# Optimization experiments

Hardware: AMD Instinct MI355X
Metric: run time of the kernel (lower is better)

Reference implementation:

```python
import jax, jax.numpy as jnp
import numpy as np

B, S, DM, H = 4, 1024, 1024, 16
DK = DM // H  # 64, must equal embeddim=64

def _linear(x, W, b):
    # torch nn.Linear: y = x @ W.T + b, W is [out, in]
    return jnp.matmul(x, W.T) + b

def setup_inputs() -> dict:
    key = jax.random.key(0)
    ks = jax.random.split(key, 40)
    inp = {}
    inp["query"] = jax.random.normal(ks[0], (B, S, DM), jnp.float32)
    inp["key"] = jax.random.normal(ks[1], (B, S, DM), jnp.float32)
    inp["value"] = jax.random.normal(ks[2], (B, S, DM), jnp.float32)
    inp["mask"] = jnp.ones((B, S, S), jnp.int32)
    def mk(i, dout, din):
        W = jax.random.normal(ks[i], (dout, din), jnp.float32) / np.sqrt(din).astype(np.float32)
        b = jax.random.normal(ks[i + 20], (dout,), jnp.float32) * 0.01
        return W, b
    # the 4 d_model x d_model projection linears (q, k, v, out)
    inp["Wq"], inp["bq"] = mk(3, DM, DM)
    inp["Wk"], inp["bk"] = mk(4, DM, DM)
    inp["Wv"], inp["bv"] = mk(5, DM, DM)
    inp["Wo"], inp["bo"] = mk(6, DM, DM)
    # the 64x64 refinement linears
    inp["Wkl"], inp["bkl"] = mk(7, DK, DK)   # key_linear
    inp["Wql"], inp["bql"] = mk(8, DK, DK)   # query_linear
    inp["Wq2"], inp["bq2"] = mk(9, DK, DK)   # query2_linear
    inp["Wvl"], inp["bvl"] = mk(10, DK, DK)  # value_linear
    inp["Wel"], inp["bel"] = mk(11, DK, DK)  # embed_linear
    return inp

def reference(query, key, value, mask,
              Wq, bq, Wk, bk, Wv, bv, Wo, bo,
              Wkl, bkl, Wql, bql, Wq2, bq2, Wvl, bvl, Wel, bel):
    b, s, dm = query.shape
    # project and split heads: [b, h, s, d_k]
    def split(x):
        return x.reshape(b, s, H, DK).transpose(0, 2, 1, 3)
    q = split(_linear(query, Wq, bq))
    k = split(_linear(key, Wk, bk))
    v = split(_linear(value, Wv, bv))
    # per-head 64x64 refinements with relu
    key_refine = jax.nn.relu(_linear(k, Wkl, bkl))
    q1 = jax.nn.relu(_linear(q, Wql, bql))
    q1 = jax.nn.relu(_linear(q1, Wel, bel))
    q2 = jax.nn.relu(_linear(q, Wq2, bq2))
    v_refine = jax.nn.relu(_linear(v, Wvl, bvl))
    # two attention-like matmuls (no 1/sqrt(d_k) scaling in original)
    qv = jnp.einsum("bhqd,bhkd->bhqk", q2, v_refine)
    kq = jnp.einsum("bhqd,bhkd->bhqk", q1, key_refine)
    m = mask[:, None, :, :]  # mask.unsqueeze(1)
    kq = jnp.where(m == 0, jnp.float32(-1e9), kq)
    attn = jax.nn.softmax(kq, axis=-1)
    # elementwise combine, then matmul against raw projected key (not value!)
    out = jnp.einsum("bhqk,bhkd->bhqd", attn * qv, k)
    out = out.transpose(0, 2, 1, 3).reshape(b, s, dm)
    return _linear(out, Wo, bo)
```

## Files before the change

kernel.cpp:

```cpp
#include <hip/hip_runtime.h>
#include <hip/hip_bf16.h>

#define B_  4
#define S_  1024
#define DM_ 1024
#define H_  16
#define DK_ 64
#define LOG2E 1.4426950408889634f

typedef unsigned short u16;
typedef __attribute__((ext_vector_type(8))) short bf16x8;
typedef __attribute__((ext_vector_type(4))) float f32x4;

__device__ __forceinline__ float bf2f(u16 u) {
    union { unsigned int i; float f; } c;
    c.i = ((unsigned int)u) << 16;
    return c.f;
}
__device__ __forceinline__ u16 f2bf(float f) {
    union { float f; unsigned int i; } c;
    c.f = f;
    unsigned int x = c.i;
    unsigned int lsb = (x >> 16) & 1u;
    x += 0x7fffu + lsb;
    return (u16)(x >> 16);
}
__device__ __forceinline__ u16 f2bf_fast(float f) {
    __hip_bfloat16 h = __float2bfloat16(f);
    return *reinterpret_cast<u16*>(&h);
}

__device__ __forceinline__ void async_ld16(const u16* g, u16* l) {
    __builtin_amdgcn_global_load_lds(
        (const __attribute__((address_space(1))) unsigned int*)(const void*)g,
        (__attribute__((address_space(3))) unsigned int*)(void*)l, 16, 0, 0);
}

__global__ void detect_kernel(const u16* __restrict__ q, int* __restrict__ flag) {
    int lane = threadIdx.x & 63;
    int cnt = 0;
#pragma unroll
    for (int i = 0; i < 4; ++i) {
        u16 u = q[2 * (lane * 4 + i)];
        int e = (u >> 7) & 0xFF;
        cnt += (e >= 100 && e <= 140) ? 1 : 0;
    }
#pragma unroll
    for (int off = 1; off < 64; off <<= 1) cnt += __shfl_xor(cnt, off, 64);
    if (lane == 0) *flag = (cnt < 128) ? 1 : 0;
}

#define NSEG 12
struct CvtArgs {
    const void* src[NSEG];
    void*       dst[NSEG];
    unsigned    off[NSEG + 1];
};

__global__ __launch_bounds__(256) void convert_kernel(
    CvtArgs a, unsigned total, const int* __restrict__ flag)
{
    if (!*flag) return;
    unsigned v = blockIdx.x * 256 + threadIdx.x;
    if (v >= total) return;
    int s = 0;
    while (s < NSEG - 1 && v >= a.off[s + 1]) ++s;
    unsigned local = v - a.off[s];
    u16* dp = (u16*)a.dst[s] + (size_t)local * 8;
    const float* sp = (const float*)a.src[s] + (size_t)local * 8;
    float4 x = *(const float4*)sp, y = *(const float4*)(sp + 4);
    u16 t[8] = {f2bf(x.x), f2bf(x.y), f2bf(x.z), f2bf(x.w),
                f2bf(y.x), f2bf(y.y), f2bf(y.z), f2bf(y.w)};
    *(uint4*)dp = *(uint4*)t;
}

__global__ __launch_bounds__(256) void maskflag_kernel(
    const int* __restrict__ mask, int* __restrict__ tflags)
{
    const int kt = blockIdx.x, b = blockIdx.y, z = blockIdx.z;
    const int tid = threadIdx.x;
    int ok = 1;
#pragma unroll
    for (int i = tid; i < 128 * 16; i += 256) {
        int row = z * 128 + (i >> 4), seg = i & 15;
        int4 m = *(const int4*)&mask[((size_t)b * S_ + row) * S_ + kt * 64 + seg * 4];
        ok &= (m.x != 0) & (m.y != 0) & (m.z != 0) & (m.w != 0);
    }
    if (!ok) atomicOr(&tflags[b * 16 + kt], 1);
}

__global__ __launch_bounds__(256) void transpose_kernel(
    const u16* __restrict__ kp, u16* __restrict__ kpt)
{
    __shared__ u16 T[64][65];
    const int s0 = blockIdx.x * 64, h = blockIdx.y, b = blockIdx.z;
    const int tid = threadIdx.x;
    const size_t base = (size_t)b * S_ * DM_ + (size_t)h * DK_;
    for (int c = tid; c < 512; c += 256) {
        int row = c >> 3, cc = (c & 7) * 8;
        union { uint4 v; u16 u[8]; } x;
        x.v = *(const uint4*)&kp[base + (size_t)(s0 + row) * DM_ + cc];
#pragma unroll
        for (int j = 0; j < 8; ++j) T[row][cc + j] = x.u[j];
    }
    __syncthreads();
    const size_t baseT = (size_t)(b * H_ + h) * DK_ * S_;
    for (int c = tid; c < 512; c += 256) {
        int d = c >> 3, ss = (c & 7) * 8;
        u16 t[8];
#pragma unroll
        for (int j = 0; j < 8; ++j) t[j] = T[ss + j][d];
        *(uint4*)&kpt[baseT + (size_t)d * S_ + s0 + ss] = *(uint4*)t;
    }
}

struct GemmBatch {
    const u16* A0[4]; const u16* A1[4];
    const u16* W0[4]; const u16* W1[4];
    const void* bias[4];
    void* C[4];
    float oscale[4];
};

template<int ACT, int BIAS_DYN, int OUT_DYN>
__global__ __launch_bounds__(256, 3) void gemm_async_kernel(
    GemmBatch gb, int M, int N, int K, const int* __restrict__ flag)
{
    __shared__ __align__(16) u16 As[128][64];
    __shared__ __align__(16) u16 Ws[128][64];

    const int g = blockIdx.z;
    const int f = *flag;
    const u16* __restrict__ A = f ? gb.A1[g] : gb.A0[g];
    const u16* __restrict__ W = f ? gb.W1[g] : gb.W0[g];
    const void* biasp = gb.bias[g];
    void* Cp = gb.C[g];

    const int m0   = blockIdx.y * 128;
    const int n0   = blockIdx.x * 128;
    const int tid  = threadIdx.x;
    const int w    = tid >> 6;
    const int lane = tid & 63;
    const int l16  = lane & 15;
    const int quad = lane >> 4;
    const int wr   = (w >> 1) * 64;
    const int wc   = (w & 1) * 64;

    const int srow = lane >> 3;
    const int sgrp = (lane & 7) ^ srow;

    f32x4 acc[4][4];
#pragma unroll
    for (int rt = 0; rt < 4; ++rt)
#pragma unroll
        for (int ct = 0; ct < 4; ++ct) acc[rt][ct] = (f32x4){0.f, 0.f, 0.f, 0.f};

    for (int k0 = 0; k0 < K; k0 += 64) {
#pragma unroll
        for (int s = 0; s < 4; ++s) {
            int seg = w * 4 + s;
            async_ld16(&A[(size_t)(m0 + seg * 8 + srow) * K + k0 + sgrp * 8],
                       &As[seg * 8][0]);
            async_ld16(&W[(size_t)(n0 + seg * 8 + srow) * K + k0 + sgrp * 8],
                       &Ws[seg * 8][0]);
        }
        __syncthreads();
#pragma unroll
        for (int kk = 0; kk < 2; ++kk) {
            const int p = (kk * 4 + quad) ^ (l16 & 7);
            bf16x8 av[4], bv[4];
#pragma unroll
            for (int rt = 0; rt < 4; ++rt)
                av[rt] = *(const bf16x8*)&As[wr + rt * 16 + l16][p * 8];
#pragma unroll
            for (int ct = 0; ct < 4; ++ct)
                bv[ct] = *(const bf16x8*)&Ws[wc + ct * 16 + l16][p * 8];
#pragma unroll
            for (int rt = 0; rt < 4; ++rt)
#pragma unroll
                for (int ct = 0; ct < 4; ++ct)
                    acc[rt][ct] = __builtin_amdgcn_mfma_f32_16x16x32_bf16(
                        av[rt], bv[ct], acc[rt][ct], 0, 0, 0);
        }
        __syncthreads();
    }

#pragma unroll
    for (int ct = 0; ct < 4; ++ct) {
        int col = n0 + wc + ct * 16 + l16;
        float bv = (BIAS_DYN && f) ? ((const float*)biasp)[col]
                                   : bf2f(((const u16*)biasp)[col]);
#pragma unroll
        for (int rt = 0; rt < 4; ++rt)
#pragma unroll
            for (int r = 0; r < 4; ++r) {
                int row = m0 + wr + rt * 16 + quad * 4 + r;
                float v = acc[rt][ct][r] + bv;
                if (ACT) v = v > 0.f ? v : 0.f;
                size_t idx = (size_t)row * N + col;
                if (OUT_DYN && f) ((float*)Cp)[idx] = v;
                else              ((u16*)Cp)[idx]   = f2bf(v);
            }
    }
}

template<int ACT, int BIAS_DYN, int OUT_DYN>
__global__ __launch_bounds__(256, 2) void gemm_small_kernel(
    GemmBatch gb, int M, int N, int K, const int* __restrict__ flag)
{
    __shared__ __align__(16) u16 As[128][72];
    __shared__ __align__(16) u16 Ws[64][72];

    const int g = blockIdx.z;
    const int f = *flag;
    const u16* __restrict__ A = f ? gb.A1[g] : gb.A0[g];
    const u16* __restrict__ W = f ? gb.W1[g] : gb.W0[g];
    const void* biasp = gb.bias[g];
    void* Cp = gb.C[g];
    const float osc = gb.oscale[g];

    const int m0   = blockIdx.y * 128;
    const int n0   = blockIdx.x * 64;
    const int tid  = threadIdx.x;
    const int w    = tid >> 6;
    const int lane = tid & 63;
    const int l16  = lane & 15;
    const int quad = lane >> 4;

    f32x4 acc[2][4];
#pragma unroll
    for (int rt = 0; rt < 2; ++rt)
#pragma unroll
        for (int ct = 0; ct < 4; ++ct) acc[rt][ct] = (f32x4){0.f, 0.f, 0.f, 0.f};

    for (int k0 = 0; k0 < K; k0 += 64) {
#pragma unroll
        for (int c = tid; c < 1024; c += 256) {
            int row = c >> 3, cc = (c & 7) * 8;
            *(uint4*)&As[row][cc] = *(const uint4*)&A[(size_t)(m0 + row) * K + k0 + cc];
        }
#pragma unroll
        for (int c = tid; c < 512; c += 256) {
            int row = c >> 3, cc = (c & 7) * 8;
            *(uint4*)&Ws[row][cc] = *(const uint4*)&W[(size_t)(n0 + row) * K + k0 + cc];
        }
        __syncthreads();
#pragma unroll
        for (int kk = 0; kk < 2; ++kk) {
            bf16x8 a[2], b[4];
#pragma unroll
            for (int rt = 0; rt < 2; ++rt)
                a[rt] = *(const bf16x8*)&As[w * 32 + rt * 16 + l16][kk * 32 + quad * 8];
#pragma unroll
            for (int ct = 0; ct < 4; ++ct)
                b[ct] = *(const bf16x8*)&Ws[ct * 16 + l16][kk * 32 + quad * 8];
#pragma unroll
            for (int rt = 0; rt < 2; ++rt)
#pragma unroll
                for (int ct = 0; ct < 4; ++ct)
                    acc[rt][ct] = __builtin_amdgcn_mfma_f32_16x16x32_bf16(
                        a[rt], b[ct], acc[rt][ct], 0, 0, 0);
        }
        __syncthreads();
    }

#pragma unroll
    for (int ct = 0; ct < 4; ++ct) {
        int col = n0 + ct * 16 + l16;
        float bv = (BIAS_DYN && f) ? ((const float*)biasp)[col]
                                   : bf2f(((const u16*)biasp)[col]);
#pragma unroll
        for (int rt = 0; rt < 2; ++rt)
#pragma unroll
            for (int r = 0; r < 4; ++r) {
                int row = m0 + w * 32 + rt * 16 + quad * 4 + r;
                float v = acc[rt][ct][r] + bv;
                if (ACT) v = v > 0.f ? v : 0.f;
                v *= osc;
                size_t idx = (size_t)row * N + col;
                if (OUT_DYN && f) ((float*)Cp)[idx] = v;
                else              ((u16*)Cp)[idx]   = f2bf(v);
            }
    }
}

__global__ __launch_bounds__(256, 2) void attn_kernel(
    const u16* __restrict__ q1, const u16* __restrict__ q2,
    const u16* __restrict__ kr, const u16* __restrict__ vr,
    const u16* __restrict__ kpt, const int* __restrict__ mask,
    const int* __restrict__ tflags, u16* __restrict__ om)
{
    __shared__ __align__(16) u16 kbuf[2][3][64][64];
    __shared__ __align__(16) u16 pts[4][32][72];

    const int qt   = blockIdx.x;
    const int h    = blockIdx.y;
    const int b    = blockIdx.z;
    const int q0   = qt * 128;
    const int tid  = threadIdx.x;
    const int w    = tid >> 6;
    const int lane = tid & 63;
    const int l16  = lane & 15;
    const int quad = lane >> 4;
    const int pb   = l16 & 7;

    const size_t base  = (size_t)b * S_ * DM_ + (size_t)h * DK_;
    const size_t baseT = (size_t)(b * H_ + h) * DK_ * S_;

    const int srow = lane >> 3;
    const int sgrp = (lane & 7) ^ srow;

    auto stage = [&](int kt, int bsel) {
        const int k0 = kt * 64;
#pragma unroll
        for (int j = 0; j < 6; ++j) {
            int idx = w * 6 + j;
            int t = idx >> 3, s = idx & 7;
            const u16* g;
            if (t == 0)      g = &kr[base + (size_t)(k0 + s * 8 + srow) * DM_ + sgrp * 8];
            else if (t == 1) g = &vr[base + (size_t)(k0 + s * 8 + srow) * DM_ + sgrp * 8];
            else             g = &kpt[baseT + (size_t)(s * 8 + srow) * S_ + k0 + sgrp * 8];
            async_ld16(g, &kbuf[bsel][t][s * 8][0]);
        }
    };

    bf16x8 a1[2][2], a2[2][2];
#pragma unroll
    for (int rt = 0; rt < 2; ++rt) {
        const int qrow = q0 + w * 32 + rt * 16 + l16;
#pragma unroll
        for (int kk = 0; kk < 2; ++kk) {
            a1[rt][kk] = *(const bf16x8*)&q1[base + (size_t)qrow * DM_ + kk * 32 + quad * 8];
            a2[rt][kk] = *(const bf16x8*)&q2[base + (size_t)qrow * DM_ + kk * 32 + quad * 8];
        }
    }

    float m_run[2][4], l_run[2][4];
    f32x4 oacc[2][4];
#pragma unroll
    for (int rt = 0; rt < 2; ++rt)
#pragma unroll
        for (int r = 0; r < 4; ++r) { m_run[rt][r] = -1e30f; l_run[rt][r] = 0.f; }
#pragma unroll
    for (int rt = 0; rt < 2; ++rt)
#pragma unroll
        for (int ct = 0; ct < 4; ++ct) oacc[rt][ct] = (f32x4){0.f, 0.f, 0.f, 0.f};

    stage(0, 0);

    for (int kt = 0; kt < S_ / 64; ++kt) {
        const int cur = kt & 1;
        const int k0 = kt * 64;
        __syncthreads();
        if (kt < S_ / 64 - 1) stage(kt + 1, cur ^ 1);

        const int tf = tflags[b * 16 + kt];

        f32x4 s1[2][4], s2[2][4];
#pragma unroll
        for (int rt = 0; rt < 2; ++rt)
#pragma unroll
            for (int ct = 0; ct < 4; ++ct) {
                s1[rt][ct] = (f32x4){0.f, 0.f, 0.f, 0.f};
                s2[rt][ct] = (f32x4){0.f, 0.f, 0.f, 0.f};
            }
#pragma unroll
        for (int kk = 0; kk < 2; ++kk) {
            bf16x8 b1[4], b2[4];
#pragma unroll
            for (int ct = 0; ct < 4; ++ct) {
                const int p = (kk * 4 + quad) ^ pb;
                b1[ct] = *(const bf16x8*)&kbuf[cur][0][ct * 16 + l16][p * 8];
                b2[ct] = *(const bf16x8*)&kbuf[cur][1][ct * 16 + l16][p * 8];
            }
#pragma unroll
            for (int rt = 0; rt < 2; ++rt)
#pragma unroll
                for (int ct = 0; ct < 4; ++ct) {
                    s1[rt][ct] = __builtin_amdgcn_mfma_f32_16x16x32_bf16(
                        a1[rt][kk], b1[ct], s1[rt][ct], 0, 0, 0);
                    s2[rt][ct] = __builtin_amdgcn_mfma_f32_16x16x32_bf16(
                        a2[rt][kk], b2[ct], s2[rt][ct], 0, 0, 0);
                }
        }

        if (tf) {
#pragma unroll
            for (int rt = 0; rt < 2; ++rt)
#pragma unroll
                for (int ct = 0; ct < 4; ++ct)
#pragma unroll
                    for (int r = 0; r < 4; ++r) {
                        int qrow = q0 + w * 32 + rt * 16 + quad * 4 + r;
                        int kc   = k0 + ct * 16 + l16;
                        if (mask[((size_t)b * S_ + qrow) * S_ + kc] == 0)
                            s1[rt][ct][r] = -1e9f;
                    }
        }

        float tmax[2][4];
#pragma unroll
        for (int rt = 0; rt < 2; ++rt)
#pragma unroll
            for (int r = 0; r < 4; ++r) tmax[rt][r] = -1e30f;
#pragma unroll
        for (int rt = 0; rt < 2; ++rt)
#pragma unroll
            for (int ct = 0; ct < 4; ++ct)
#pragma unroll
                for (int r = 0; r < 4; ++r)
                    tmax[rt][r] = fmaxf(tmax[rt][r], s1[rt][ct][r]);
#pragma unroll
        for (int off = 1; off < 16; off <<= 1)
#pragma unroll
            for (int rt = 0; rt < 2; ++rt)
#pragma unroll
                for (int r = 0; r < 4; ++r)
                    tmax[rt][r] = fmaxf(tmax[rt][r], __shfl_xor(tmax[rt][r], off, 64));

        float alpha[2][4], newm[2][4];
#pragma unroll
        for (int rt = 0; rt < 2; ++rt)
#pragma unroll
            for (int r = 0; r < 4; ++r) {
                newm[rt][r]  = fmaxf(m_run[rt][r], tmax[rt][r]);
                alpha[rt][r] = exp2f(m_run[rt][r] - newm[rt][r]);
                m_run[rt][r] = newm[rt][r];
            }

        float psum[2][4] = {};
#pragma unroll
        for (int rt = 0; rt < 2; ++rt)
#pragma unroll
            for (int ct = 0; ct < 4; ++ct)
#pragma unroll
                for (int r = 0; r < 4; ++r) {
                    float p = exp2f(s1[rt][ct][r] - newm[rt][r]);
                    psum[rt][r] += p;
                    pts[w][rt * 16 + quad * 4 + r][ct * 16 + l16] =
                        f2bf_fast(p * s2[rt][ct][r]);
                }
#pragma unroll
        for (int off = 1; off < 16; off <<= 1)
#pragma unroll
            for (int rt = 0; rt < 2; ++rt)
#pragma unroll
                for (int r = 0; r < 4; ++r)
                    psum[rt][r] += __shfl_xor(psum[rt][r], off, 64);
#pragma unroll
        for (int rt = 0; rt < 2; ++rt)
#pragma unroll
            for (int r = 0; r < 4; ++r)
                l_run[rt][r] = l_run[rt][r] * alpha[rt][r] + psum[rt][r];
#pragma unroll
        for (int rt = 0; rt < 2; ++rt)
#pragma unroll
            for (int ct = 0; ct < 4; ++ct)
#pragma unroll
                for (int r = 0; r < 4; ++r) oacc[rt][ct][r] *= alpha[rt][r];

        {
            bf16x8 bb[2][4];
#pragma unroll
            for (int kk = 0; kk < 2; ++kk)
#pragma unroll
                for (int ct = 0; ct < 4; ++ct) {
                    const int p = (kk * 4 + quad) ^ pb;
                    bb[kk][ct] = *(const bf16x8*)&kbuf[cur][2][ct * 16 + l16][p * 8];
                }
#pragma unroll
            for (int rt = 0; rt < 2; ++rt)
#pragma unroll
                for (int kk = 0; kk < 2; ++kk) {
                    bf16x8 a = *(const bf16x8*)&pts[w][rt * 16 + l16][kk * 32 + quad * 8];
#pragma unroll
                    for (int ct = 0; ct < 4; ++ct)
                        oacc[rt][ct] = __builtin_amdgcn_mfma_f32_16x16x32_bf16(
                            a, bb[kk][ct], oacc[rt][ct], 0, 0, 0);
                }
        }
    }

#pragma unroll
    for (int rt = 0; rt < 2; ++rt)
#pragma unroll
        for (int ct = 0; ct < 4; ++ct)
#pragma unroll
            for (int r = 0; r < 4; ++r) {
                int row = q0 + w * 32 + rt * 16 + quad * 4 + r;
                int col = ct * 16 + l16;
                float v = oacc[rt][ct][r] / l_run[rt][r];
                om[base + (size_t)row * DM_ + col] = f2bf_fast(v);
            }
}

extern "C" void kernel_launch(void* const* d_in, const int* in_sizes, int n_in,
                              void* d_out, int out_size, void* d_ws, size_t ws_size,
                              hipStream_t stream)
{
    const void* query = d_in[0];
    const void* key   = d_in[1];
    const void* value = d_in[2];
    const int*  mask  = (const int*)d_in[3];
    const void* Wq  = d_in[4];  const void* bq  = d_in[5];
    const void* Wk  = d_in[6];  const void* bk  = d_in[7];
    const void* Wv  = d_in[8];  const void* bv  = d_in[9];
    const void* Wo  = d_in[10]; const void* bo  = d_in[11];
    const void* Wkl = d_in[12]; const void* bkl = d_in[13];
    const void* Wql = d_in[14]; const void* bql = d_in[15];
    const void* Wq2 = d_in[16]; const void* bq2 = d_in[17];
    const void* Wvl = d_in[18]; const void* bvl = d_in[19];
    const void* Wel = d_in[20]; const void* bel = d_in[21];

    int* flag   = (int*)d_ws;
    int* tflags = (int*)d_ws + 4;
    u16* ws     = (u16*)((char*)d_ws + 512);
    const size_t BUF = (size_t)(B_ * S_) * DM_;
    u16* Qp  = ws + 0 * BUF;
    u16* Kp  = ws + 1 * BUF;
    u16* Vp  = ws + 2 * BUF;
    u16* krb = ws + 3 * BUF;
    u16* q1a = ws + 4 * BUF;
    u16* q1b = ws + 5 * BUF;
    u16* q2r = ws + 6 * BUF;
    u16* vrb = ws + 7 * BUF;
    u16* Om  = ws + 8 * BUF;
    u16* Qc  = ws + 9 * BUF;
    u16* Kc  = ws + 10 * BUF;
    u16* Vc  = ws + 11 * BUF;
    u16* Wbig = ws + 12 * BUF;
    u16* Wqc = Wbig + 0 * (size_t)(DM_ * DM_);
    u16* Wkc = Wbig + 1 * (size_t)(DM_ * DM_);
    u16* Wvc = Wbig + 2 * (size_t)(DM_ * DM_);
    u16* Woc = Wbig + 3 * (size_t)(DM_ * DM_);
    u16* Wsm = Wbig + 4 * (size_t)(DM_ * DM_);
    u16* Wklc = Wsm + 0 * (DK_ * DK_);
    u16* Wqlc = Wsm + 1 * (DK_ * DK_);
    u16* Welc = Wsm + 2 * (DK_ * DK_);
    u16* Wq2c = Wsm + 3 * (DK_ * DK_);
    u16* Wvlc = Wsm + 4 * (DK_ * DK_);
    u16* KpT = Vp;

    const int M = B_ * S_;
    dim3 blk(256);

    detect_kernel<<<1, 64, 0, stream>>>((const u16*)query, flag);

    CvtArgs ca;
    const unsigned VIN = (unsigned)(BUF / 8);
    const unsigned VWB = (unsigned)(DM_ * DM_ / 8);
    const unsigned VWS = (unsigned)(DK_ * DK_ / 8);
    const void* srcs[NSEG] = {query, key, value, Wq, Wk, Wv, Wo, Wkl, Wql, Wel, Wq2, Wvl};
    void* dsts[NSEG] = {Qc, Kc, Vc, Wqc, Wkc, Wvc, Woc, Wklc, Wqlc, Welc, Wq2c, Wvlc};
    unsigned vcn[NSEG] = {VIN, VIN, VIN, VWB, VWB, VWB, VWB, VWS, VWS, VWS, VWS, VWS};
    unsigned off = 0;
    for (int i = 0; i < NSEG; ++i) { ca.src[i] = srcs[i]; ca.dst[i] = dsts[i]; ca.off[i] = off; off += vcn[i]; }
    ca.off[NSEG] = off;
    convert_kernel<<<dim3((off + 255) / 256), blk, 0, stream>>>(ca, off, flag);

    hipMemsetAsync(tflags, 0, 64 * sizeof(int), stream);
    maskflag_kernel<<<dim3(16, 4, 8), blk, 0, stream>>>(mask, tflags);

    GemmBatch gqkv = {};
    gqkv.A0[0] = (const u16*)query; gqkv.A1[0] = Qc;
    gqkv.A0[1] = (const u16*)key;   gqkv.A1[1] = Kc;
    gqkv.A0[2] = (const u16*)value; gqkv.A1[2] = Vc;
    gqkv.W0[0] = (const u16*)Wq; gqkv.W1[0] = Wqc;
    gqkv.W0[1] = (const u16*)Wk; gqkv.W1[1] = Wkc;
    gqkv.W0[2] = (const u16*)Wv; gqkv.W1[2] = Wvc;
    gqkv.bias[0] = bq; gqkv.bias[1] = bk; gqkv.bias[2] = bv;
    gqkv.C[0] = Qp; gqkv.C[1] = Kp; gqkv.C[2] = Vp;
    dim3 gBig(DM_ / 128, M / 128, 3);
    gemm_async_kernel<0,1,0><<<gBig, blk, 0, stream>>>(gqkv, M, DM_, DM_, flag);

    GemmBatch gref = {};
    gref.A0[0] = gref.A1[0] = Kp; gref.W0[0] = (const u16*)Wkl; gref.W1[0] = Wklc;
    gref.A0[1] = gref.A1[1] = Qp; gref.W0[1] = (const u16*)Wql; gref.W1[1] = Wqlc;
    gref.A0[2] = gref.A1[2] = Qp; gref.W0[2] = (const u16*)Wq2; gref.W1[2] = Wq2c;
    gref.A0[3] = gref.A1[3] = Vp; gref.W0[3] = (const u16*)Wvl; gref.W1[3] = Wvlc;
    gref.bias[0] = bkl; gref.bias[1] = bql; gref.bias[2] = bq2; gref.bias[3] = bvl;
    gref.C[0] = krb; gref.C[1] = q1a; gref.C[2] = q2r; gref.C[3] = vrb;
    gref.oscale[0] = gref.oscale[1] = gref.oscale[2] = gref.oscale[3] = 1.0f;
    dim3 gSm(1, (M * H_) / 128, 4);
    gemm_small_kernel<1,1,0><<<gSm, blk, 0, stream>>>(gref, M * H_, DK_, DK_, flag);

    GemmBatch gel = {};
    gel.A0[0] = gel.A1[0] = q1a; gel.W0[0] = (const u16*)Wel; gel.W1[0] = Welc;
    gel.bias[0] = bel; gel.C[0] = q1b; gel.oscale[0] = LOG2E;
    dim3 gS1(1, (M * H_) / 128, 1);
    gemm_small_kernel<1,1,0><<<gS1, blk, 0, stream>>>(gel, M * H_, DK_, DK_, flag);

    dim3 gT(S_ / 64, H_, B_);
    transpose_kernel<<<gT, blk, 0, stream>>>(Kp, KpT);

    dim3 gA(S_ / 128, H_, B_);
    attn_kernel<<<gA, blk, 0, stream>>>(q1b, q2r, krb, vrb, KpT, mask, tflags, Om);

    GemmBatch go = {};
    go.A0[0] = go.A1[0] = Om; go.W0[0] = (const u16*)Wo; go.W1[0] = Woc;
    go.bias[0] = bo; go.C[0] = (u16*)d_out;
    dim3 gO(DM_ / 128, M / 128, 1);
    gemm_async_kernel<0,1,1><<<gO, blk, 0, stream>>>(go, M, DM_, DM_, flag);
}
```

Measured before the change: 330.8 us.

## Fuse mask-flag scan into convert kernel, chain q1 refinements, simplify attn staging

Merges the mask tile scan into the conversion kernel as extra blocks, removing one launch. Chains the query_linear and embed_linear 64x64 GEMMs inside one small-GEMM block so the intermediate q1 stays in shared memory instead of making a global round trip. Also replaces the attention kernel's double-buffered async swizzled K/V staging with synchronous padded-LDS loads, which drops load/compute overlap in exchange for simpler code.

```diff
diff --git a/kernel.cpp b/kernel.cpp
--- a/kernel.cpp
+++ b/kernel.cpp
@@ -57,11 +57,26 @@
     unsigned    off[NSEG + 1];
 };
 
-__global__ __launch_bounds__(256) void convert_kernel(
-    CvtArgs a, unsigned total, const int* __restrict__ flag)
+__global__ __launch_bounds__(256) void prep_kernel(
+    CvtArgs a, unsigned total, const int* __restrict__ flag,
+    const int* __restrict__ mask, int* __restrict__ tflags)
 {
+    const int tid = threadIdx.x;
+    if (blockIdx.x < 512) {
+        const int bx = blockIdx.x;
+        const int kt = bx & 15, b = (bx >> 4) & 3, z = bx >> 6;
+        int ok = 1;
+#pragma unroll
+        for (int i = tid; i < 128 * 16; i += 256) {
+            int row = z * 128 + (i >> 4), seg = i & 15;
+            int4 m = *(const int4*)&mask[((size_t)b * S_ + row) * S_ + kt * 64 + seg * 4];
+            ok &= (m.x != 0) & (m.y != 0) & (m.z != 0) & (m.w != 0);
+        }
+        if (!ok) atomicOr(&tflags[b * 16 + kt], 1);
+        return;
+    }
     if (!*flag) return;
-    unsigned v = blockIdx.x * 256 + threadIdx.x;
+    unsigned v = (blockIdx.x - 512) * 256 + tid;
     if (v >= total) return;
     int s = 0;
     while (s < NSEG - 1 && v >= a.off[s + 1]) ++s;
@@ -72,21 +87,6 @@
     u16 t[8] = {f2bf(x.x), f2bf(x.y), f2bf(x.z), f2bf(x.w),
                 f2bf(y.x), f2bf(y.y), f2bf(y.z), f2bf(y.w)};
     *(uint4*)dp = *(uint4*)t;
-}
-
-__global__ __launch_bounds__(256) void maskflag_kernel(
-    const int* __restrict__ mask, int* __restrict__ tflags)
-{
-    const int kt = blockIdx.x, b = blockIdx.y, z = blockIdx.z;
-    const int tid = threadIdx.x;
-    int ok = 1;
-#pragma unroll
-    for (int i = tid; i < 128 * 16; i += 256) {
-        int row = z * 128 + (i >> 4), seg = i & 15;
-        int4 m = *(const int4*)&mask[((size_t)b * S_ + row) * S_ + kt * 64 + seg * 4];
-        ok &= (m.x != 0) & (m.y != 0) & (m.z != 0) & (m.w != 0);
-    }
-    if (!ok) atomicOr(&tflags[b * 16 + kt], 1);
 }
 
 __global__ __launch_bounds__(256) void transpose_kernel(
@@ -117,9 +117,12 @@
 struct GemmBatch {
     const u16* A0[4]; const u16* A1[4];
     const u16* W0[4]; const u16* W1[4];
+    const u16* W20[4]; const u16* W21[4];
     const void* bias[4];
+    const void* bias2[4];
     void* C[4];
     float oscale[4];
+    int chain[4];
 };
 
 template<int ACT, int BIAS_DYN, int OUT_DYN>
@@ -218,6 +221,7 @@
     const void* biasp = gb.bias[g];
     void* Cp = gb.C[g];
     const float osc = gb.oscale[g];
+    const int chain = gb.chain[g];
 
     const int m0   = blockIdx.y * 128;
     const int n0   = blockIdx.x * 64;
@@ -264,23 +268,85 @@
         __syncthreads();
     }
 
-#pragma unroll
-    for (int ct = 0; ct < 4; ++ct) {
-        int col = n0 + ct * 16 + l16;
-        float bv = (BIAS_DYN && f) ? ((const float*)biasp)[col]
-                                   : bf2f(((const u16*)biasp)[col]);
-#pragma unroll
-        for (int rt = 0; rt < 2; ++rt)
-#pragma unroll
-            for (int r = 0; r < 4; ++r) {
-                int row = m0 + w * 32 + rt * 16 + quad * 4 + r;
-                float v = acc[rt][ct][r] + bv;
-                if (ACT) v = v > 0.f ? v : 0.f;
-                v *= osc;
-                size_t idx = (size_t)row * N + col;
-                if (OUT_DYN && f) ((float*)Cp)[idx] = v;
-                else              ((u16*)Cp)[idx]   = f2bf(v);
-            }
+    if (!chain) {
+#pragma unroll
+        for (int ct = 0; ct < 4; ++ct) {
+            int col = n0 + ct * 16 + l16;
+            float bv = (BIAS_DYN && f) ? ((const float*)biasp)[col]
+                                       : bf2f(((const u16*)biasp)[col]);
+#pragma unroll
+            for (int rt = 0; rt < 2; ++rt)
+#pragma unroll
+                for (int r = 0; r < 4; ++r) {
+                    int row = m0 + w * 32 + rt * 16 + quad * 4 + r;
+                    float v = acc[rt][ct][r] + bv;
+                    if (ACT) v = v > 0.f ? v : 0.f;
+                    v *= osc;
+                    size_t idx = (size_t)row * N + col;
+                    if (OUT_DYN && f) ((float*)Cp)[idx] = v;
+                    else              ((u16*)Cp)[idx]   = f2bf(v);
+                }
+        }
+    } else {
+        const u16* __restrict__ W2 = f ? gb.W21[g] : gb.W20[g];
+#pragma unroll
+        for (int c = tid; c < 512; c += 256) {
+            int row = c >> 3, cc = (c & 7) * 8;
+            *(uint4*)&Ws[row][cc] = *(const uint4*)&W2[(size_t)row * 64 + cc];
+        }
+#pragma unroll
+        for (int ct = 0; ct < 4; ++ct) {
+            int col = ct * 16 + l16;
+            float bv = (BIAS_DYN && f) ? ((const float*)biasp)[col]
+                                       : bf2f(((const u16*)biasp)[col]);
+#pragma unroll
+            for (int rt = 0; rt < 2; ++rt)
+#pragma unroll
+                for (int r = 0; r < 4; ++r) {
+                    float v = acc[rt][ct][r] + bv;
+                    v = v > 0.f ? v : 0.f;
+                    As[w * 32 + rt * 16 + quad * 4 + r][col] = f2bf(v);
+                }
+        }
+        __syncthreads();
+
+        f32x4 acc2[2][4];
+#pragma unroll
+        for (int rt = 0; rt < 2; ++rt)
+#pragma unroll
+            for (int ct = 0; ct < 4; ++ct) acc2[rt][ct] = (f32x4){0.f, 0.f, 0.f, 0.f};
+#pragma unroll
+        for (int kk = 0; kk < 2; ++kk) {
+            bf16x8 a[2], b[4];
+#pragma unroll
+            for (int rt = 0; rt < 2; ++rt)
+                a[rt] = *(const bf16x8*)&As[w * 32 + rt * 16 + l16][kk * 32 + quad * 8];
+#pragma unroll
+            for (int ct = 0; ct < 4; ++ct)
+                b[ct] = *(const bf16x8*)&Ws[ct * 16 + l16][kk * 32 + quad * 8];
+#pragma unroll
+            for (int rt = 0; rt < 2; ++rt)
+#pragma unroll
+                for (int ct = 0; ct < 4; ++ct)
+                    acc2[rt][ct] = __builtin_amdgcn_mfma_f32_16x16x32_bf16(
+                        a[rt], b[ct], acc2[rt][ct], 0, 0, 0);
+        }
+#pragma unroll
+        for (int ct = 0; ct < 4; ++ct) {
+            int col = ct * 16 + l16;
+            float bv2 = (BIAS_DYN && f) ? ((const float*)gb.bias2[g])[col]
+                                        : bf2f(((const u16*)gb.bias2[g])[col]);
+#pragma unroll
+            for (int rt = 0; rt < 2; ++rt)
+#pragma unroll
+                for (int r = 0; r < 4; ++r) {
+                    int row = m0 + w * 32 + rt * 16 + quad * 4 + r;
+                    float v = acc2[rt][ct][r] + bv2;
+                    v = v > 0.f ? v : 0.f;
+                    v *= osc;
+                    ((u16*)Cp)[(size_t)row * N + col] = f2bf(v);
+                }
+        }
     }
 }
 
@@ -290,7 +356,9 @@
     const u16* __restrict__ kpt, const int* __restrict__ mask,
     const int* __restrict__ tflags, u16* __restrict__ om)
 {
-    __shared__ __align__(16) u16 kbuf[2][3][64][64];
+    __shared__ __align__(16) u16 krs[64][72];
+    __shared__ __align__(16) u16 vrs[64][72];
+    __shared__ __align__(16) u16 kts[64][72];
     __shared__ __align__(16) u16 pts[4][32][72];
 
     const int qt   = blockIdx.x;
@@ -302,27 +370,9 @@
     const int lane = tid & 63;
     const int l16  = lane & 15;
     const int quad = lane >> 4;
-    const int pb   = l16 & 7;
 
     const size_t base  = (size_t)b * S_ * DM_ + (size_t)h * DK_;
     const size_t baseT = (size_t)(b * H_ + h) * DK_ * S_;
-
-    const int srow = lane >> 3;
-    const int sgrp = (lane & 7) ^ srow;
-
-    auto stage = [&](int kt, int bsel) {
-        const int k0 = kt * 64;
-#pragma unroll
-        for (int j = 0; j < 6; ++j) {
-            int idx = w * 6 + j;
-            int t = idx >> 3, s = idx & 7;
-            const u16* g;
-            if (t == 0)      g = &kr[base + (size_t)(k0 + s * 8 + srow) * DM_ + sgrp * 8];
-            else if (t == 1) g = &vr[base + (size_t)(k0 + s * 8 + srow) * DM_ + sgrp * 8];
-            else             g = &kpt[baseT + (size_t)(s * 8 + srow) * S_ + k0 + sgrp * 8];
-            async_ld16(g, &kbuf[bsel][t][s * 8][0]);
-        }
-    };
 
     bf16x8 a1[2][2], a2[2][2];
 #pragma unroll
@@ -346,13 +396,16 @@
 #pragma unroll
         for (int ct = 0; ct < 4; ++ct) oacc[rt][ct] = (f32x4){0.f, 0.f, 0.f, 0.f};
 
-    stage(0, 0);
-
     for (int kt = 0; kt < S_ / 64; ++kt) {
-        const int cur = kt & 1;
         const int k0 = kt * 64;
         __syncthreads();
-        if (kt < S_ / 64 - 1) stage(kt + 1, cur ^ 1);
+        for (int c = tid; c < 512; c += 256) {
+            int row = c >> 3, cc = (c & 7) * 8;
+            *(uint4*)&krs[row][cc] = *(const uint4*)&kr[base + (size_t)(k0 + row) * DM_ + cc];
+            *(uint4*)&vrs[row][cc] = *(const uint4*)&vr[base + (size_t)(k0 + row) * DM_ + cc];
+            *(uint4*)&kts[row][cc] = *(const uint4*)&kpt[baseT + (size_t)row * S_ + k0 + cc];
+        }
+        __syncthreads();
 
         const int tf = tflags[b * 16 + kt];
 
@@ -369,9 +422,8 @@
             bf16x8 b1[4], b2[4];
 #pragma unroll
             for (int ct = 0; ct < 4; ++ct) {
-                const int p = (kk * 4 + quad) ^ pb;
-                b1[ct] = *(const bf16x8*)&kbuf[cur][0][ct * 16 + l16][p * 8];
-                b2[ct] = *(const bf16x8*)&kbuf[cur][1][ct * 16 + l16][p * 8];
+                b1[ct] = *(const bf16x8*)&krs[ct * 16 + l16][kk * 32 + quad * 8];
+                b2[ct] = *(const bf16x8*)&vrs[ct * 16 + l16][kk * 32 + quad * 8];
             }
 #pragma unroll
             for (int rt = 0; rt < 2; ++rt)
@@ -464,10 +516,8 @@
 #pragma unroll
             for (int kk = 0; kk < 2; ++kk)
 #pragma unroll
-                for (int ct = 0; ct < 4; ++ct) {
-                    const int p = (kk * 4 + quad) ^ pb;
-                    bb[kk][ct] = *(const bf16x8*)&kbuf[cur][2][ct * 16 + l16][p * 8];
-                }
+                for (int ct = 0; ct < 4; ++ct)
+                    bb[kk][ct] = *(const bf16x8*)&kts[ct * 16 + l16][kk * 32 + quad * 8];
 #pragma unroll
             for (int rt = 0; rt < 2; ++rt)
 #pragma unroll
@@ -520,15 +570,14 @@
     u16* Kp  = ws + 1 * BUF;
     u16* Vp  = ws + 2 * BUF;
     u16* krb = ws + 3 * BUF;
-    u16* q1a = ws + 4 * BUF;
-    u16* q1b = ws + 5 * BUF;
-    u16* q2r = ws + 6 * BUF;
-    u16* vrb = ws + 7 * BUF;
-    u16* Om  = ws + 8 * BUF;
-    u16* Qc  = ws + 9 * BUF;
-    u16* Kc  = ws + 10 * BUF;
-    u16* Vc  = ws + 11 * BUF;
-    u16* Wbig = ws + 12 * BUF;
+    u16* q1b = ws + 4 * BUF;
+    u16* q2r = ws + 5 * BUF;
+    u16* vrb = ws + 6 * BUF;
+    u16* Om  = ws + 7 * BUF;
+    u16* Qc  = ws + 8 * BUF;
+    u16* Kc  = ws + 9 * BUF;
+    u16* Vc  = ws + 10 * BUF;
+    u16* Wbig = ws + 11 * BUF;
     u16* Wqc = Wbig + 0 * (size_t)(DM_ * DM_);
     u16* Wkc = Wbig + 1 * (size_t)(DM_ * DM_);
     u16* Wvc = Wbig + 2 * (size_t)(DM_ * DM_);
@@ -546,6 +595,7 @@
 
     detect_kernel<<<1, 64, 0, stream>>>((const u16*)query, flag);
 
+    hipMemsetAsync(tflags, 0, 64 * sizeof(int), stream);
     CvtArgs ca;
     const unsigned VIN = (unsigned)(BUF / 8);
     const unsigned VWB = (unsigned)(DM_ * DM_ / 8);
@@ -556,10 +606,7 @@
     unsigned off = 0;
     for (int i = 0; i < NSEG; ++i) { ca.src[i] = srcs[i]; ca.dst[i] = dsts[i]; ca.off[i] = off; off += vcn[i]; }
     ca.off[NSEG] = off;
-    convert_kernel<<<dim3((off + 255) / 256), blk, 0, stream>>>(ca, off, flag);
-
-    hipMemsetAsync(tflags, 0, 64 * sizeof(int), stream);
-    maskflag_kernel<<<dim3(16, 4, 8), blk, 0, stream>>>(mask, tflags);
+    prep_kernel<<<dim3(512 + (off + 255) / 256), blk, 0, stream>>>(ca, off, flag, mask, tflags);
 
     GemmBatch gqkv = {};
     gqkv.A0[0] = (const u16*)query; gqkv.A1[0] = Qc;
@@ -579,16 +626,12 @@
     gref.A0[2] = gref.A1[2] = Qp; gref.W0[2] = (const u16*)Wq2; gref.W1[2] = Wq2c;
     gref.A0[3] = gref.A1[3] = Vp; gref.W0[3] = (const u16*)Wvl; gref.W1[3] = Wvlc;
     gref.bias[0] = bkl; gref.bias[1] = bql; gref.bias[2] = bq2; gref.bias[3] = bvl;
-    gref.C[0] = krb; gref.C[1] = q1a; gref.C[2] = q2r; gref.C[3] = vrb;
-    gref.oscale[0] = gref.oscale[1] = gref.oscale[2] = gref.oscale[3] = 1.0f;
+    gref.C[0] = krb; gref.C[1] = q1b; gref.C[2] = q2r; gref.C[3] = vrb;
+    gref.oscale[0] = 1.0f; gref.oscale[1] = LOG2E; gref.oscale[2] = 1.0f; gref.oscale[3] = 1.0f;
+    gref.chain[0] = 0; gref.chain[1] = 1; gref.chain[2] = 0; gref.chain[3] = 0;
+    gref.W20[1] = (const u16*)Wel; gref.W21[1] = Welc; gref.bias2[1] = bel;
     dim3 gSm(1, (M * H_) / 128, 4);
     gemm_small_kernel<1,1,0><<<gSm, blk, 0, stream>>>(gref, M * H_, DK_, DK_, flag);
-
-    GemmBatch gel = {};
-    gel.A0[0] = gel.A1[0] = q1a; gel.W0[0] = (const u16*)Wel; gel.W1[0] = Welc;
-    gel.bias[0] = bel; gel.C[0] = q1b; gel.oscale[0] = LOG2E;
-    dim3 gS1(1, (M * H_) / 128, 1);
-    gemm_small_kernel<1,1,0><<<gS1, blk, 0, stream>>>(gel, M * H_, DK_, DK_, flag);
 
     dim3 gT(S_ / 64, H_, B_);
     transpose_kernel<<<gT, blk, 0, stream>>>(Kp, KpT);
```

After: 316.7 us. -4.3%, faster.
